# Kernel tuning notes

Measured on AMD Instinct MI355X. Metric: run time of the kernel, lower is better.

## Reference

```python
import jax, jax.numpy as jnp
import numpy as np

L, B, N_IN, N_OUT, BIDIR, K = 2048, 16, 256, 256, 2, 6


def setup_inputs() -> dict:
    key = jax.random.key(0)
    k1, k2 = jax.random.split(key, 2)
    x = jax.random.normal(k1, (L, B, N_IN), jnp.float32)
    val = (6.0 / (N_IN + N_OUT)) ** 0.5
    weight_in = jax.random.uniform(k2, (N_IN, BIDIR * N_OUT * K), jnp.float32, -val, val)
    bias_in = jnp.zeros((K * BIDIR * N_OUT,), jnp.float32)
    c1_init = jnp.zeros((B, BIDIR * N_OUT), jnp.float32)
    c2_init = jnp.zeros((B, BIDIR * N_OUT), jnp.float32)
    d_init = jnp.zeros((B, BIDIR * N_OUT), jnp.float32)
    return {"x": x, "weight_in": weight_in, "bias_in": bias_in,
            "c1_init": c1_init, "c2_init": c2_init, "d_init": d_init}


def _flip_dir1(a):
    # reverse time for the backward direction (dir index 1)
    return a.at[:, :, 1].set(jnp.flip(a[:, :, 1], axis=0))


def _sopa_forward(x, weight_in, bias_in, c1_init, c2_init, d_init):
    length, batch = x.shape[0], x.shape[1]
    # u_: [L, B, bidir, n_out, k]
    u = (x.reshape(-1, N_IN) @ weight_in).reshape(length, batch, BIDIR, N_OUT, K)
    bias = bias_in.reshape(K, BIDIR, N_OUT)  # [k, bidir, n_out]
    x1, x2, x3 = u[..., 0], u[..., 1], u[..., 2]
    f1 = jax.nn.sigmoid(u[..., 3] + bias[3])
    f2 = jax.nn.sigmoid(u[..., 4] + bias[4])
    # selfloop gate sigmoid(u[...,5]+bias[5]) is computed in the original but
    # unused by the recurrence, so it is omitted here (no effect on outputs).

    # flip time for direction 1 so one scan handles both directions
    x1f, x2f, x3f, f1f, f2f = (_flip_dir1(a) for a in (x1, x2, x3, f1, f2))

    c1_0 = c1_init.reshape(batch, BIDIR, N_OUT)
    c2_0 = c2_init.reshape(batch, BIDIR, N_OUT)
    d_0 = d_init.reshape(batch, BIDIR, N_OUT)

    def step(carry, inp):
        c1, c2, d = carry
        x1t, x2t, x3t, f1t, f2t = inp
        c1n = (c1 - x1t) * f1t + x1t
        tmp = x3t * d
        c2n = (c2 - tmp) * f2t + tmp
        return (c1n, c2n, x2t), (c1n, c2n)

    (c1_f, c2_f, d_f), (c1s, c2s) = jax.lax.scan(
        step, (c1_0, c2_0, d_0), (x1f, x2f, x3f, f1f, f2f))

    c1s = _flip_dir1(c1s)
    c2s = _flip_dir1(c2s)
    return (c1s, c2s,
            c1_f.reshape(batch, -1), c2_f.reshape(batch, -1), d_f.reshape(batch, -1))


def reference(x, weight_in, bias_in, c1_init, c2_init, d_init):
    return _sopa_forward(x, weight_in, bias_in, c1_init, c2_init, d_init)
```

## Files before the change

### kernel.cpp

```cpp
#include <hip/hip_runtime.h>
#include <cstdint>
#include <cstddef>

typedef unsigned short u16;
typedef unsigned int u32;
typedef __bf16 bf16x8 __attribute__((ext_vector_type(8)));
typedef float f32x4 __attribute__((ext_vector_type(4)));

#define SL 2048
#define NCH 8192
#define SEGS 64

#define OFF_C2S 16777216
#define OFF_C1F 33554432
#define OFF_C2F 33562624
#define OFF_DF  33570816

__device__ __forceinline__ u16 f2bf(float f) {
  union { float f; u32 i; } v; v.f = f;
  u32 x = v.i;
  return (u16)((x + 0x7fffu + ((x >> 16) & 1u)) >> 16);
}
__device__ __forceinline__ u32 cvtpk(float lo, float hi) {
  u32 r;
  asm("v_cvt_pk_bf16_f32 %0, %1, %2" : "=v"(r) : "v"(lo), "v"(hi));
  return r;
}
__device__ __forceinline__ float sigmoidf(float v) {
  return 1.f / (1.f + __expf(-v));
}

__global__ __launch_bounds__(256) void xconv_kernel(
    const float* __restrict__ x, u16* __restrict__ xb) {
  int t8 = blockIdx.x * 256 + threadIdx.x;
  int kb = t8 & 31;
  int b  = (t8 >> 5) & 15;
  int ot = t8 >> 9;
  const float* src = x + (((size_t)(ot * 16 + b)) << 8) + kb * 8;
  f32x4 a = *(const f32x4*)src;
  f32x4 c = *(const f32x4*)(src + 4);
  union { bf16x8 v; u32 u[4]; } h;
  h.u[0] = cvtpk(a[0], a[1]);
  h.u[1] = cvtpk(a[2], a[3]);
  h.u[2] = cvtpk(c[0], c[1]);
  h.u[3] = cvtpk(c[2], c[3]);
  *(bf16x8*)(xb + ((size_t)ot << 12) + kb * 128 + b * 8) = h.v;
}

__global__ __launch_bounds__(256) void repack_kernel(
    const float* __restrict__ W, u16* __restrict__ Wt) {
  int idx = blockIdx.x * 256 + threadIdx.x;
  int kk8 = idx & 7;
  int lane = (idx >> 3) & 63;
  int h  = (idx >> 9) & 1;
  int kt = (idx >> 10) & 3;
  int cg = (idx >> 12) & 31;
  int p  = idx >> 17;
  int ch2 = cg * 16 + (lane & 15);
  int kk  = (kt * 8 + h * 4 + (lane >> 4)) * 8 + kk8;
  Wt[idx] = f2bf(W[(size_t)kk * 3072 + (ch2 >> 8) * 1536 + (ch2 & 255) * 6 + p]);
}

__global__ __launch_bounds__(256, 2) void fusedA_kernel(
    const u16* __restrict__ xb, const u16* __restrict__ Wt,
    const float* __restrict__ bias,
    float* __restrict__ A1, float* __restrict__ B1,
    float* __restrict__ A2, float* __restrict__ B2k,
    float* __restrict__ G2, float* __restrict__ X2B) {
  const int tid = threadIdx.x;
  const int lane = tid & 63;
  const int wc = tid >> 6;
  const int l15 = lane & 15, l4 = lane >> 4;
  const int s = blockIdx.x;
  const int bc = blockIdx.y;
  const int dir = bc >> 2;
  const int ch2 = bc * 64 + wc * 16 + l15;
  const int fb0 = (bc * 4 + wc) * 8;

  const float bv3 = bias[1536 + ch2];
  const float bv4 = bias[2048 + ch2];

  float a1[4], b1[4], a2[4], b2[4], g2[4], x2p[4];
#pragma unroll
  for (int r = 0; r < 4; ++r) {
    a1[r] = 1.f; b1[r] = 0.f; a2[r] = 1.f; b2[r] = 0.f;
    g2[r] = 0.f; x2p[r] = 0.f;
  }

  for (int rt = 0; rt < 8; ++rt) {
    const u16* ab0; const u16* ab1; const u16* ab2; const u16* ab3;
    {
      int tf = s * 32 + rt * 4;
      int o0 = dir ? (SL - 1 - tf) : tf;
      int o1 = dir ? (o0 - 1) : (o0 + 1);
      int o2 = dir ? (o0 - 2) : (o0 + 2);
      int o3 = dir ? (o0 - 3) : (o0 + 3);
      size_t lo = (size_t)(l4 * 128 + l15 * 8);
      ab0 = xb + ((size_t)o0 << 12) + lo;
      ab1 = xb + ((size_t)o1 << 12) + lo;
      ab2 = xb + ((size_t)o2 << 12) + lo;
      ab3 = xb + ((size_t)o3 << 12) + lo;
    }

    f32x4 acc[5][4];
#pragma unroll
    for (int p = 0; p < 5; ++p)
#pragma unroll
      for (int i = 0; i < 4; ++i) acc[p][i] = (f32x4){0.f, 0.f, 0.f, 0.f};

#pragma unroll
    for (int kt = 0; kt < 4; ++kt) {
#pragma unroll
      for (int h = 0; h < 2; ++h) {
        const int kb4 = (kt * 8 + h * 4) * 128;
        bf16x8 af[4];
        af[0] = *(const bf16x8*)(ab0 + kb4);
        af[1] = *(const bf16x8*)(ab1 + kb4);
        af[2] = *(const bf16x8*)(ab2 + kb4);
        af[3] = *(const bf16x8*)(ab3 + kb4);
        const int fb = fb0 + kt * 2 + h;
#pragma unroll
        for (int p = 0; p < 5; ++p) {
          bf16x8 bfr = *(const bf16x8*)(
              Wt + (size_t)(p * 256 + fb) * 512 + lane * 8);
#pragma unroll
          for (int i = 0; i < 4; ++i)
            acc[p][i] = __builtin_amdgcn_mfma_f32_16x16x32_bf16(
                af[i], bfr, acc[p][i], 0, 0, 0);
        }
      }
    }

    const bool first = (rt == 0);
#pragma unroll
    for (int i = 0; i < 4; ++i) {
#pragma unroll
      for (int r = 0; r < 4; ++r) {
        float x1 = acc[0][i][r], x2v = acc[1][i][r], x3 = acc[2][i][r];
        float f1 = sigmoidf(acc[3][i][r] + bv3);
        float f2 = sigmoidf(acc[4][i][r] + bv4);
        a1[r] *= f1;
        b1[r] = f1 * b1[r] + (1.f - f1) * x1;
        float tmp = x3 * x2p[r];
        a2[r] *= f2;
        b2[r] = f2 * b2[r] + (1.f - f2) * tmp;
        g2[r] = (first && i == 0) ? (1.f - f2) * x3 : g2[r] * f2;
        x2p[r] = x2v;
      }
    }
  }

  const int chb = (l4 * 4) * 512 + ch2;
  const size_t o = (size_t)s * NCH + chb;
#pragma unroll
  for (int r = 0; r < 4; ++r) {
    size_t oo = o + (size_t)r * 512;
    A1[oo] = a1[r]; B1[oo] = b1[r]; A2[oo] = a2[r];
    B2k[oo] = b2[r]; G2[oo] = g2[r]; X2B[oo] = x2p[r];
  }
}

__global__ __launch_bounds__(256) void scanB_kernel(
    const float* __restrict__ A1, const float* __restrict__ B1,
    const float* __restrict__ A2, const float* __restrict__ B2k,
    const float* __restrict__ G2, const float* __restrict__ X2B,
    const float* __restrict__ c1_init, const float* __restrict__ c2_init,
    const float* __restrict__ d_init,
    float* __restrict__ C1c, float* __restrict__ C2c,
    float* __restrict__ out) {
  int ch = blockIdx.x * 256 + threadIdx.x;
  float c1 = c1_init[ch], c2 = c2_init[ch], d0 = d_init[ch];
#pragma unroll 8
  for (int s = 0; s < SEGS; ++s) {
    int o = s * NCH + ch;
    C1c[o] = c1; C2c[o] = c2;
    c1 = A1[o] * c1 + B1[o];
    c2 = A2[o] * c2 + (B2k[o] + G2[o] * d0);
    d0 = X2B[o];
  }
  out[OFF_C1F + ch] = c1;
  out[OFF_C2F + ch] = c2;
  out[OFF_DF + ch] = d0;
}

__global__ __launch_bounds__(256, 2) void fusedC_kernel(
    const u16* __restrict__ xb, const u16* __restrict__ Wt,
    const float* __restrict__ bias, const float* __restrict__ d_init,
    const float* __restrict__ X2B,
    const float* __restrict__ C1c, const float* __restrict__ C2c,
    float* __restrict__ out) {
  const int tid = threadIdx.x;
  const int lane = tid & 63;
  const int wc = tid >> 6;
  const int l15 = lane & 15, l4 = lane >> 4;
  const int s = blockIdx.x;
  const int bc = blockIdx.y;
  const int dir = bc >> 2;
  const int ch2 = bc * 64 + wc * 16 + l15;
  const int fb0 = (bc * 4 + wc) * 8;

  const float bv3 = bias[1536 + ch2];
  const float bv4 = bias[2048 + ch2];

  const int chb = (l4 * 4) * 512 + ch2;
  float c1[4], c2[4], x2p[4];
  {
    size_t o = (size_t)s * NCH + chb;
#pragma unroll
    for (int r = 0; r < 4; ++r) {
      c1[r] = C1c[o + r * 512];
      c2[r] = C2c[o + r * 512];
      x2p[r] = (s == 0) ? d_init[chb + r * 512] : X2B[o - NCH + r * 512];
    }
  }

  for (int rt = 0; rt < 8; ++rt) {
    const u16* ab0; const u16* ab1; const u16* ab2; const u16* ab3;
    {
      int tf = s * 32 + rt * 4;
      int o0 = dir ? (SL - 1 - tf) : tf;
      int o1 = dir ? (o0 - 1) : (o0 + 1);
      int o2 = dir ? (o0 - 2) : (o0 + 2);
      int o3 = dir ? (o0 - 3) : (o0 + 3);
      size_t lo = (size_t)(l4 * 128 + l15 * 8);
      ab0 = xb + ((size_t)o0 << 12) + lo;
      ab1 = xb + ((size_t)o1 << 12) + lo;
      ab2 = xb + ((size_t)o2 << 12) + lo;
      ab3 = xb + ((size_t)o3 << 12) + lo;
    }

    f32x4 acc[5][4];
#pragma unroll
    for (int p = 0; p < 5; ++p)
#pragma unroll
      for (int i = 0; i < 4; ++i) acc[p][i] = (f32x4){0.f, 0.f, 0.f, 0.f};

#pragma unroll
    for (int kt = 0; kt < 4; ++kt) {
#pragma unroll
      for (int h = 0; h < 2; ++h) {
        const int kb4 = (kt * 8 + h * 4) * 128;
        bf16x8 af[4];
        af[0] = *(const bf16x8*)(ab0 + kb4);
        af[1] = *(const bf16x8*)(ab1 + kb4);
        af[2] = *(const bf16x8*)(ab2 + kb4);
        af[3] = *(const bf16x8*)(ab3 + kb4);
        const int fb = fb0 + kt * 2 + h;
#pragma unroll
        for (int p = 0; p < 5; ++p) {
          bf16x8 bfr = *(const bf16x8*)(
              Wt + (size_t)(p * 256 + fb) * 512 + lane * 8);
#pragma unroll
          for (int i = 0; i < 4; ++i)
            acc[p][i] = __builtin_amdgcn_mfma_f32_16x16x32_bf16(
                af[i], bfr, acc[p][i], 0, 0, 0);
        }
      }
    }

#pragma unroll
    for (int i = 0; i < 4; ++i) {
      int tfl = s * 32 + rt * 4 + i;
      int t_out = dir ? (SL - 1 - tfl) : tfl;
      float* orow = out + (size_t)t_out * NCH + chb;
#pragma unroll
      for (int r = 0; r < 4; ++r) {
        float x1 = acc[0][i][r], x2v = acc[1][i][r], x3 = acc[2][i][r];
        float f1 = sigmoidf(acc[3][i][r] + bv3);
        float f2 = sigmoidf(acc[4][i][r] + bv4);
        c1[r] = f1 * c1[r] + (1.f - f1) * x1;
        float tmp = x3 * x2p[r];
        c2[r] = f2 * c2[r] + (1.f - f2) * tmp;
        x2p[r] = x2v;
        __builtin_nontemporal_store(c1[r], orow + r * 512);
        __builtin_nontemporal_store(c2[r], orow + OFF_C2S + (size_t)r * 512);
      }
    }
  }
}

extern "C" void kernel_launch(void* const* d_in, const int* in_sizes, int n_in,
                              void* d_out, int out_size, void* d_ws, size_t ws_size,
                              hipStream_t stream) {
  const float* x    = (const float*)d_in[0];
  const float* W    = (const float*)d_in[1];
  const float* bias = (const float*)d_in[2];
  const float* c1i  = (const float*)d_in[3];
  const float* c2i  = (const float*)d_in[4];
  const float* di   = (const float*)d_in[5];
  float* out = (float*)d_out;

  uint8_t* w8 = (uint8_t*)d_ws;
  u16* Wt  = (u16*)w8;
  u16* xb  = (u16*)(w8 + 1310720ull);
  float* X2B = (float*)(w8 + 18087936ull);
  float* A1  = (float*)(w8 + 20185088ull);
  float* B1  = A1  + SEGS * NCH;
  float* A2  = B1  + SEGS * NCH;
  float* B2k = A2  + SEGS * NCH;
  float* G2  = B2k + SEGS * NCH;
  float* C1c = G2  + SEGS * NCH;
  float* C2c = C1c + SEGS * NCH;

  hipLaunchKernelGGL(xconv_kernel, dim3(4096), dim3(256), 0, stream, x, xb);
  hipLaunchKernelGGL(repack_kernel, dim3(2560), dim3(256), 0, stream, W, Wt);
  hipLaunchKernelGGL(fusedA_kernel, dim3(64, 8), dim3(256), 0, stream,
                     xb, Wt, bias, A1, B1, A2, B2k, G2, X2B);
  hipLaunchKernelGGL(scanB_kernel, dim3(32), dim3(256), 0, stream,
                     A1, B1, A2, B2k, G2, X2B, c1i, c2i, di, C1c, C2c, out);
  hipLaunchKernelGGL(fusedC_kernel, dim3(64, 8), dim3(256), 0, stream,
                     xb, Wt, bias, di, X2B, C1c, C2c, out);
}
```

Before: 370.3 us.

## Coalesce preprocessing, vectorize segment-state I/O, and remap blocks across XCDs

xconv now reads x in the order its output is laid out, and repack now reads W coalesced and scatters the writes, skipping the unused gate column. The per-segment state arrays (A1, B1, A2, B2k, G2, X2B, C1c, C2c) move to a [seg][ch2][batch] layout, so fusedA and fusedC write and read them with float4 accesses and scanB reads them with a matching index. The 2D grids become 1D with a block-to-(segment, channel-group) mapping that keeps consecutive segments on the same XCD, aiming for better L2 locality. The cost is scattered writes in repack and an index permutation that must stay consistent across all three kernels.

```diff
diff --git a/kernel.cpp b/kernel.cpp
--- a/kernel.cpp
+++ b/kernel.cpp
@@ -33,8 +33,8 @@
 __global__ __launch_bounds__(256) void xconv_kernel(
     const float* __restrict__ x, u16* __restrict__ xb) {
   int t8 = blockIdx.x * 256 + threadIdx.x;
-  int kb = t8 & 31;
-  int b  = (t8 >> 5) & 15;
+  int b  = t8 & 15;
+  int kb = (t8 >> 4) & 31;
   int ot = t8 >> 9;
   const float* src = x + (((size_t)(ot * 16 + b)) << 8) + kb * 8;
   f32x4 a = *(const f32x4*)src;
@@ -50,15 +50,21 @@
 __global__ __launch_bounds__(256) void repack_kernel(
     const float* __restrict__ W, u16* __restrict__ Wt) {
   int idx = blockIdx.x * 256 + threadIdx.x;
-  int kk8 = idx & 7;
-  int lane = (idx >> 3) & 63;
-  int h  = (idx >> 9) & 1;
-  int kt = (idx >> 10) & 3;
-  int cg = (idx >> 12) & 31;
-  int p  = idx >> 17;
-  int ch2 = cg * 16 + (lane & 15);
-  int kk  = (kt * 8 + h * 4 + (lane >> 4)) * 8 + kk8;
-  Wt[idx] = f2bf(W[(size_t)kk * 3072 + (ch2 >> 8) * 1536 + (ch2 & 255) * 6 + p]);
+  int col = idx % 3072;
+  int kk  = idx / 3072;
+  float w = W[idx];
+  int d    = (col >= 1536) ? 1 : 0;
+  int col2 = col - d * 1536;
+  int n = col2 / 6;
+  int p = col2 - n * 6;
+  if (p >= 5) return;
+  int ch2 = d * 256 + n;
+  int cg = ch2 >> 4, l15 = ch2 & 15;
+  int kk8 = kk & 7, q = kk >> 3;
+  int l4 = q & 3, h = (q >> 2) & 1, kt = q >> 3;
+  size_t dst = ((size_t)(p * 256 + cg * 8 + kt * 2 + h)) * 512 +
+               (l4 * 16 + l15) * 8 + kk8;
+  Wt[dst] = f2bf(w);
 }
 
 __global__ __launch_bounds__(256, 2) void fusedA_kernel(
@@ -71,8 +77,11 @@
   const int lane = tid & 63;
   const int wc = tid >> 6;
   const int l15 = lane & 15, l4 = lane >> 4;
-  const int s = blockIdx.x;
-  const int bc = blockIdx.y;
+  const int bid = blockIdx.x;
+  const int xcd = bid & 7;
+  const int j = bid >> 3;
+  const int s = xcd * 8 + (j & 7);
+  const int bc = j >> 3;
   const int dir = bc >> 2;
   const int ch2 = bc * 64 + wc * 16 + l15;
   const int fb0 = (bc * 4 + wc) * 8;
@@ -150,14 +159,13 @@
     }
   }
 
-  const int chb = (l4 * 4) * 512 + ch2;
-  const size_t o = (size_t)s * NCH + chb;
-#pragma unroll
-  for (int r = 0; r < 4; ++r) {
-    size_t oo = o + (size_t)r * 512;
-    A1[oo] = a1[r]; B1[oo] = b1[r]; A2[oo] = a2[r];
-    B2k[oo] = b2[r]; G2[oo] = g2[r]; X2B[oo] = x2p[r];
-  }
+  const size_t oo = (size_t)s * NCH + (size_t)ch2 * 16 + l4 * 4;
+  *(f32x4*)(A1  + oo) = (f32x4){a1[0], a1[1], a1[2], a1[3]};
+  *(f32x4*)(B1  + oo) = (f32x4){b1[0], b1[1], b1[2], b1[3]};
+  *(f32x4*)(A2  + oo) = (f32x4){a2[0], a2[1], a2[2], a2[3]};
+  *(f32x4*)(B2k + oo) = (f32x4){b2[0], b2[1], b2[2], b2[3]};
+  *(f32x4*)(G2  + oo) = (f32x4){g2[0], g2[1], g2[2], g2[3]};
+  *(f32x4*)(X2B + oo) = (f32x4){x2p[0], x2p[1], x2p[2], x2p[3]};
 }
 
 __global__ __launch_bounds__(256) void scanB_kernel(
@@ -168,11 +176,13 @@
     const float* __restrict__ d_init,
     float* __restrict__ C1c, float* __restrict__ C2c,
     float* __restrict__ out) {
-  int ch = blockIdx.x * 256 + threadIdx.x;
+  int t = blockIdx.x * 256 + threadIdx.x;
+  int ch2 = t >> 4, b = t & 15;
+  int ch = b * 512 + ch2;
   float c1 = c1_init[ch], c2 = c2_init[ch], d0 = d_init[ch];
 #pragma unroll 8
   for (int s = 0; s < SEGS; ++s) {
-    int o = s * NCH + ch;
+    int o = s * NCH + t;
     C1c[o] = c1; C2c[o] = c2;
     c1 = A1[o] * c1 + B1[o];
     c2 = A2[o] * c2 + (B2k[o] + G2[o] * d0);
@@ -193,8 +203,11 @@
   const int lane = tid & 63;
   const int wc = tid >> 6;
   const int l15 = lane & 15, l4 = lane >> 4;
-  const int s = blockIdx.x;
-  const int bc = blockIdx.y;
+  const int bid = blockIdx.x;
+  const int xcd = bid & 7;
+  const int j = bid >> 3;
+  const int s = xcd * 8 + (j & 7);
+  const int bc = j >> 3;
   const int dir = bc >> 2;
   const int ch2 = bc * 64 + wc * 16 + l15;
   const int fb0 = (bc * 4 + wc) * 8;
@@ -205,12 +218,18 @@
   const int chb = (l4 * 4) * 512 + ch2;
   float c1[4], c2[4], x2p[4];
   {
-    size_t o = (size_t)s * NCH + chb;
-#pragma unroll
-    for (int r = 0; r < 4; ++r) {
-      c1[r] = C1c[o + r * 512];
-      c2[r] = C2c[o + r * 512];
-      x2p[r] = (s == 0) ? d_init[chb + r * 512] : X2B[o - NCH + r * 512];
+    const size_t oo = (size_t)s * NCH + (size_t)ch2 * 16 + l4 * 4;
+    f32x4 u0 = *(const f32x4*)(C1c + oo);
+    f32x4 w0 = *(const f32x4*)(C2c + oo);
+#pragma unroll
+    for (int r = 0; r < 4; ++r) { c1[r] = u0[r]; c2[r] = w0[r]; }
+    if (s == 0) {
+#pragma unroll
+      for (int r = 0; r < 4; ++r) x2p[r] = d_init[chb + r * 512];
+    } else {
+      f32x4 xv = *(const f32x4*)(X2B + oo - NCH);
+#pragma unroll
+      for (int r = 0; r < 4; ++r) x2p[r] = xv[r];
     }
   }
 
@@ -303,11 +322,11 @@
   float* C2c = C1c + SEGS * NCH;
 
   hipLaunchKernelGGL(xconv_kernel, dim3(4096), dim3(256), 0, stream, x, xb);
-  hipLaunchKernelGGL(repack_kernel, dim3(2560), dim3(256), 0, stream, W, Wt);
-  hipLaunchKernelGGL(fusedA_kernel, dim3(64, 8), dim3(256), 0, stream,
+  hipLaunchKernelGGL(repack_kernel, dim3(3072), dim3(256), 0, stream, W, Wt);
+  hipLaunchKernelGGL(fusedA_kernel, dim3(512), dim3(256), 0, stream,
                      xb, Wt, bias, A1, B1, A2, B2k, G2, X2B);
   hipLaunchKernelGGL(scanB_kernel, dim3(32), dim3(256), 0, stream,
                      A1, B1, A2, B2k, G2, X2B, c1i, c2i, di, C1c, C2c, out);
-  hipLaunchKernelGGL(fusedC_kernel, dim3(64, 8), dim3(256), 0, stream,
+  hipLaunchKernelGGL(fusedC_kernel, dim3(512), dim3(256), 0, stream,
                      xb, Wt, bias, di, X2B, C1c, C2c, out);
 }
```

Measured after the change: 363.3 us. No clear change (-1.9%).
